# Kernel optimization log

Measured on AMD Instinct MI355X. Metric: run time of the kernel, lower is better.

The kernel has to match this reference:

```python
import jax, jax.numpy as jnp
import numpy as np

B, N, C_IN = 8, 8192, 64
M, K, RADIUS = 1024, 64, 0.2
MLP = [64, 64, 128]


def _fps(pts, m):
    """Iterative farthest point sampling. pts: [N,3] -> [m] int32 indices."""
    n = pts.shape[0]

    def step(carry, _):
        dists, last = carry
        d = jnp.sum((pts - pts[last]) ** 2, axis=-1)          # [N]
        dists = jnp.minimum(dists, d)
        nxt = jnp.argmax(dists).astype(jnp.int32)
        return (dists, nxt), nxt

    init = (jnp.full((n,), 1e10, pts.dtype), jnp.int32(0))
    _, idx = jax.lax.scan(step, init, None, length=m - 1)
    return jnp.concatenate([jnp.zeros((1,), jnp.int32), idx])


def _ball_query(new_xyz, xyz, radius, k):
    """new_xyz: [B,3,M], xyz: [B,3,N] -> [B,M,K] neighbor indices.
    First k points within radius (in index order); padded with first hit."""
    d2 = (jnp.sum(new_xyz ** 2, 1)[:, :, None] + jnp.sum(xyz ** 2, 1)[:, None, :]
          - 2.0 * jnp.einsum('bcm,bcn->bmn', new_xyz, xyz))   # [B,M,N]
    mask = d2 < radius * radius
    # stable argsort of ~mask puts indices of in-radius points first, in order
    order = jnp.argsort(jnp.where(mask, 0, 1).astype(jnp.int32), axis=-1)[..., :k]
    count = jnp.sum(mask, axis=-1)                             # [B,M]
    valid = jnp.arange(k)[None, None, :] < count[..., None]
    return jnp.where(valid, order, order[..., :1])


def _group(x, idx):
    """x: [B,C,N], idx: [B,...] -> [B,C,...] gathered along N."""
    return jax.vmap(lambda a, i: a[:, i])(x, idx)


def _forward(xyz, feature, params):
    # FPS centroid indices (torch runs under no_grad -> stop_gradient)
    pts = jax.lax.stop_gradient(jnp.transpose(xyz, (0, 2, 1)))  # [B,N,3]
    cidx = jax.vmap(lambda p: _fps(p, M))(pts)                  # [B,M]
    new_xyz = _group(xyz, cidx)                                 # [B,3,M]
    nidx = _ball_query(jax.lax.stop_gradient(new_xyz),
                       jax.lax.stop_gradient(xyz), RADIUS, K)   # [B,M,K]
    gxyz = _group(xyz, nidx) - new_xyz[..., None]               # [B,3,M,K]
    x = jnp.concatenate([gxyz, _group(feature, nidx)], axis=1)  # [B,3+C,M,K]
    # SharedMLP: 1x1 conv2d + BN (folded to per-channel scale/bias) + ReLU
    for w, s, b in params:
        x = jax.nn.relu(jnp.einsum('oi,bimk->bomk', w, x)
                        * s[:, None, None] + b[:, None, None])
    return new_xyz, jnp.max(x, axis=3)                          # [B,3,M], [B,128,M]


def setup_inputs() -> dict:
    key = jax.random.key(0)
    ks = jax.random.split(key, 5)
    inp = {
        'xyz': jax.random.normal(ks[0], (B, 3, N), jnp.float32),
        'feature': jax.random.normal(ks[1], (B, C_IN, N), jnp.float32),
    }
    prev = C_IN + 3  # use_xyz=True
    for li, co in enumerate(MLP):
        inp[f'w{li}'] = jax.random.normal(ks[2 + li], (co, prev), jnp.float32) / np.sqrt(prev).astype(np.float32)
        inp[f's{li}'] = jnp.ones((co,), jnp.float32)
        inp[f'b{li}'] = jnp.zeros((co,), jnp.float32)
        prev = co
    return inp


def reference(xyz, feature, w0, s0, b0, w1, s1, b1, w2, s2, b2):
    return _forward(xyz, feature, ((w0, s0, b0), (w1, s1, b1), (w2, s2, b2)))
```

## Files before the change

### kernel.cpp

```cpp
#include <hip/hip_runtime.h>


#define B_ 8
#define N_ 8192
#define M_ 1024
#define K_ 64
#define FTW 68

template <int CTRL>
__device__ __forceinline__ unsigned long long dpp_key(unsigned long long k) {
  int lo = __builtin_amdgcn_update_dpp(0, (int)(unsigned int)k, CTRL, 0xF, 0xF, true);
  int hi = __builtin_amdgcn_update_dpp(0, (int)(unsigned int)(k >> 32), CTRL, 0xF, 0xF, true);
  unsigned long long o = ((unsigned long long)(unsigned int)hi << 32) | (unsigned int)lo;
  return o > k ? o : k;
}

template <int CTRL>
__device__ __forceinline__ float dpp_fmax(float v) {
  int o = __builtin_amdgcn_update_dpp(0, __float_as_int(v), CTRL, 0xF, 0xF, true);
  return fmaxf(v, __int_as_float(o));
}
__device__ __forceinline__ float wave_fmax63(float v) {
  v = dpp_fmax<0xB1>(v);
  v = dpp_fmax<0x4E>(v);
  v = dpp_fmax<0x141>(v);
  v = dpp_fmax<0x140>(v);
  v = dpp_fmax<0x142>(v);
  v = dpp_fmax<0x143>(v);
  return v;
}

__global__ __launch_bounds__(256, 1) void fps_ft_kernel(const float* __restrict__ xyz,
                                                        const float* __restrict__ feat,
                                                        float* __restrict__ ft,
                                                        float* __restrict__ nxyz) {
#pragma clang fp contract(off)
  if (blockIdx.x >= 8) {
    const int nb = gridDim.x - 8;
    const int total = B_ * N_ * FTW;
    for (int idx = (blockIdx.x - 8) * 256 + threadIdx.x; idx < total; idx += nb * 256) {
      int c = idx % FTW;
      int bn = idx / FTW;
      int n = bn & (N_ - 1);
      int b = bn >> 13;
      float v;
      if (c < 3) v = xyz[(b * 3 + c) * N_ + n];
      else if (c < 67) v = feat[(b * 64 + (c - 3)) * N_ + n];
      else v = 0.f;
      ft[idx] = v;
    }
    return;
  }

  __shared__ float4 pts4[N_];
  __shared__ unsigned long long cand[2][16];
  __shared__ int scidx[M_];
  const int b = blockIdx.x;
  const int t = threadIdx.x;
  const int lane = t & 63;
  const int wid = t >> 6;
  const float* xb = xyz + b * 3 * N_;

  for (int n = t; n < N_; n += 256) {
    pts4[n] = make_float4(xb[n], xb[N_ + n], xb[2 * N_ + n], 0.f);
  }

  const int base = t * 32;
  float px[32], py[32], pz[32], mind[32];
#pragma unroll
  for (int j = 0; j < 32; ++j) {
    px[j] = xb[base + j];
    py[j] = xb[N_ + base + j];
    pz[j] = xb[2 * N_ + base + j];
    mind[j] = 1e10f;
  }
  float xl = xb[0], yl = xb[N_], zl = xb[2 * N_];
  if (t == 0) scidx[0] = 0;
  __syncthreads();

  for (int i = 1; i < M_; ++i) {
    float bestv = -1.f;
    int bl = 0;
#pragma unroll
    for (int j = 0; j < 32; ++j) {
      float dx = __fsub_rn(px[j], xl);
      float dy = __fsub_rn(py[j], yl);
      float dz = __fsub_rn(pz[j], zl);
      float d = __fadd_rn(__fadd_rn(__fmul_rn(dx, dx), __fmul_rn(dy, dy)), __fmul_rn(dz, dz));
      float md = fminf(mind[j], d);
      mind[j] = md;
      if (md > bestv) { bestv = md; bl = j; }
    }
    unsigned long long key =
        ((unsigned long long)__float_as_uint(bestv) << 32) | (unsigned int)(~(base + bl));
    key = dpp_key<0xB1>(key);
    key = dpp_key<0x4E>(key);
    key = dpp_key<0x141>(key);
    key = dpp_key<0x140>(key);
    if ((lane & 15) == 0) cand[i & 1][wid * 4 + (lane >> 4)] = key;
    __syncthreads();
    unsigned long long gk = cand[i & 1][lane & 15];
    gk = dpp_key<0xB1>(gk);
    gk = dpp_key<0x4E>(gk);
    gk = dpp_key<0x141>(gk);
    gk = dpp_key<0x140>(gk);
    const int gi = (int)(~(unsigned int)gk);
    if (t == 0) scidx[i] = gi;
    float4 cc = pts4[gi];
    xl = cc.x; yl = cc.y; zl = cc.z;
  }
  __syncthreads();
  for (int q = t; q < M_; q += 256) {
    int ci = scidx[q];
    float4 c = pts4[ci];
    nxyz[b * 3 * M_ + q] = c.x;
    nxyz[b * 3 * M_ + M_ + q] = c.y;
    nxyz[b * 3 * M_ + 2 * M_ + q] = c.z;
  }
}

__global__ __launch_bounds__(256) void ballq_kernel(const float* __restrict__ xyz,
                                                    const float* __restrict__ nxyz,
                                                    int* __restrict__ nidx) {
  const int lane = threadIdx.x & 63;
  const int g = blockIdx.x * 4 + (threadIdx.x >> 6);
  const int b = g >> 10;
  const int m = g & (M_ - 1);
  const float* xb = xyz + b * 3 * N_;
  const float cx = nxyz[b * 3 * M_ + m];
  const float cy = nxyz[b * 3 * M_ + M_ + m];
  const float cz = nxyz[b * 3 * M_ + 2 * M_ + m];
  const float nc = __fadd_rn(__fadd_rn(__fmul_rn(cx, cx), __fmul_rn(cy, cy)), __fmul_rn(cz, cz));
  int cnt = 0;
  int first = 0;
  int* slot = nidx + (g << 6);
  for (int basei = 0; basei < N_ && cnt < K_; basei += 64) {
    const int n = basei + lane;
    float p_x = xb[n], p_y = xb[N_ + n], p_z = xb[2 * N_ + n];
    float pn = __fadd_rn(__fadd_rn(__fmul_rn(p_x, p_x), __fmul_rn(p_y, p_y)), __fmul_rn(p_z, p_z));
    float dt = __fadd_rn(__fadd_rn(__fmul_rn(cx, p_x), __fmul_rn(cy, p_y)), __fmul_rn(cz, p_z));
    float d2 = __fsub_rn(__fadd_rn(nc, pn), __fmul_rn(2.f, dt));
    bool inr = d2 < 0.04f;
    unsigned long long mk = __ballot(inr);
    if (cnt == 0 && mk != 0ull) first = basei + (__ffsll((long long)mk) - 1);
    int pos = cnt + (int)__popcll(mk & ((1ull << lane) - 1ull));
    if (inr && pos < K_) slot[pos] = n;
    cnt += (int)__popcll(mk);
  }
  if (cnt > K_) cnt = K_;
  if (lane >= cnt) slot[lane] = first;
}

template <bool USE_FT>
__global__ __launch_bounds__(64, 4) void mlp_kernel(
    const float* __restrict__ ft, const float* __restrict__ xyz, const float* __restrict__ feat,
    const int* __restrict__ nidx, const float* __restrict__ nxyz,
    const float* __restrict__ w0, const float* __restrict__ s0, const float* __restrict__ b0,
    const float* __restrict__ w1, const float* __restrict__ s1, const float* __restrict__ b1,
    const float* __restrict__ w2, const float* __restrict__ s2, const float* __restrict__ b2,
    float* __restrict__ out2) {
  __shared__ float ylds[64 * 33];
  const int g = blockIdx.x;
  const int b = g >> 10;
  const int m = g & (M_ - 1);
  const int lane = threadIdx.x;
  const int n = nidx[(g << 6) + lane];
  const float cx = nxyz[b * 3 * M_ + m];
  const float cy = nxyz[b * 3 * M_ + M_ + m];
  const float cz = nxyz[b * 3 * M_ + 2 * M_ + m];

  float x0[67];
  if (USE_FT) {
    const float4* row = (const float4*)(ft + (size_t)((b << 13) + n) * FTW);
    float f[FTW];
#pragma unroll
    for (int q = 0; q < 17; ++q) {
      float4 v = row[q];
      f[q * 4 + 0] = v.x; f[q * 4 + 1] = v.y; f[q * 4 + 2] = v.z; f[q * 4 + 3] = v.w;
    }
    x0[0] = f[0] - cx; x0[1] = f[1] - cy; x0[2] = f[2] - cz;
#pragma unroll
    for (int c = 3; c < 67; ++c) x0[c] = f[c];
  } else {
    const float* xb = xyz + b * 3 * N_;
    x0[0] = xb[n] - cx; x0[1] = xb[N_ + n] - cy; x0[2] = xb[2 * N_ + n] - cz;
#pragma unroll
    for (int c = 0; c < 64; ++c) x0[3 + c] = feat[((b << 6) + c) * N_ + n];
  }

  float x1[64];
#pragma unroll
  for (int h = 0; h < 2; ++h) {
#pragma unroll 2
    for (int oo = 0; oo < 32; oo += 4) {
      const int o = h * 32 + oo;
      const float* wr = w0 + o * 67;
      float a0 = 0.f, a1 = 0.f, a2 = 0.f, a3 = 0.f;
#pragma unroll
      for (int ci = 0; ci < 67; ++ci) {
        float xvv = x0[ci];
        a0 = fmaf(wr[ci], xvv, a0);
        a1 = fmaf(wr[67 + ci], xvv, a1);
        a2 = fmaf(wr[134 + ci], xvv, a2);
        a3 = fmaf(wr[201 + ci], xvv, a3);
      }
      ylds[lane * 33 + oo + 0] = fmaxf(fmaf(a0, s0[o + 0], b0[o + 0]), 0.f);
      ylds[lane * 33 + oo + 1] = fmaxf(fmaf(a1, s0[o + 1], b0[o + 1]), 0.f);
      ylds[lane * 33 + oo + 2] = fmaxf(fmaf(a2, s0[o + 2], b0[o + 2]), 0.f);
      ylds[lane * 33 + oo + 3] = fmaxf(fmaf(a3, s0[o + 3], b0[o + 3]), 0.f);
    }
#pragma unroll
    for (int c = 0; c < 32; ++c) x1[h * 32 + c] = ylds[lane * 33 + c];
  }

  float x2[64];
#pragma unroll
  for (int h = 0; h < 2; ++h) {
#pragma unroll 2
    for (int oo = 0; oo < 32; oo += 4) {
      const int o = h * 32 + oo;
      const float* wr = w1 + o * 64;
      float a0 = 0.f, a1 = 0.f, a2 = 0.f, a3 = 0.f;
#pragma unroll
      for (int ci = 0; ci < 64; ++ci) {
        float xvv = x1[ci];
        a0 = fmaf(wr[ci], xvv, a0);
        a1 = fmaf(wr[64 + ci], xvv, a1);
        a2 = fmaf(wr[128 + ci], xvv, a2);
        a3 = fmaf(wr[192 + ci], xvv, a3);
      }
      ylds[lane * 33 + oo + 0] = fmaxf(fmaf(a0, s1[o + 0], b1[o + 0]), 0.f);
      ylds[lane * 33 + oo + 1] = fmaxf(fmaf(a1, s1[o + 1], b1[o + 1]), 0.f);
      ylds[lane * 33 + oo + 2] = fmaxf(fmaf(a2, s1[o + 2], b1[o + 2]), 0.f);
      ylds[lane * 33 + oo + 3] = fmaxf(fmaf(a3, s1[o + 3], b1[o + 3]), 0.f);
    }
#pragma unroll
    for (int c = 0; c < 32; ++c) x2[h * 32 + c] = ylds[lane * 33 + c];
  }

  float* outbm = out2 + (size_t)(b * 128) * M_ + m;
#pragma unroll 2
  for (int o = 0; o < 128; o += 4) {
    const float* wr = w2 + o * 64;
    float a0 = 0.f, a1 = 0.f, a2 = 0.f, a3 = 0.f;
#pragma unroll
    for (int ci = 0; ci < 64; ++ci) {
      float xvv = x2[ci];
      a0 = fmaf(wr[ci], xvv, a0);
      a1 = fmaf(wr[64 + ci], xvv, a1);
      a2 = fmaf(wr[128 + ci], xvv, a2);
      a3 = fmaf(wr[192 + ci], xvv, a3);
    }
    float v0 = fmaxf(fmaf(a0, s2[o + 0], b2[o + 0]), 0.f);
    float v1 = fmaxf(fmaf(a1, s2[o + 1], b2[o + 1]), 0.f);
    float v2 = fmaxf(fmaf(a2, s2[o + 2], b2[o + 2]), 0.f);
    float v3 = fmaxf(fmaf(a3, s2[o + 3], b2[o + 3]), 0.f);
    v0 = wave_fmax63(v0);
    v1 = wave_fmax63(v1);
    v2 = wave_fmax63(v2);
    v3 = wave_fmax63(v3);
    float g0 = __int_as_float(__builtin_amdgcn_readlane(__float_as_int(v0), 63));
    float g1 = __int_as_float(__builtin_amdgcn_readlane(__float_as_int(v1), 63));
    float g2 = __int_as_float(__builtin_amdgcn_readlane(__float_as_int(v2), 63));
    float g3 = __int_as_float(__builtin_amdgcn_readlane(__float_as_int(v3), 63));
    if (lane == ((o + 0) & 63)) outbm[(o + 0) * M_] = g0;
    if (lane == ((o + 1) & 63)) outbm[(o + 1) * M_] = g1;
    if (lane == ((o + 2) & 63)) outbm[(o + 2) * M_] = g2;
    if (lane == ((o + 3) & 63)) outbm[(o + 3) * M_] = g3;
  }
}

extern "C" void kernel_launch(void* const* d_in, const int* in_sizes, int n_in,
                              void* d_out, int out_size, void* d_ws, size_t ws_size,
                              hipStream_t stream) {
  const float* xyz = (const float*)d_in[0];
  const float* feat = (const float*)d_in[1];
  const float* w0 = (const float*)d_in[2];
  const float* s0 = (const float*)d_in[3];
  const float* b0 = (const float*)d_in[4];
  const float* w1 = (const float*)d_in[5];
  const float* s1 = (const float*)d_in[6];
  const float* b1 = (const float*)d_in[7];
  const float* w2 = (const float*)d_in[8];
  const float* s2 = (const float*)d_in[9];
  const float* b2 = (const float*)d_in[10];

  float* nxyz = (float*)d_out;
  float* out2 = (float*)d_out + B_ * 3 * M_;

  const size_t nidx_bytes = (size_t)B_ * M_ * K_ * sizeof(int);
  const size_t ft_bytes = (size_t)B_ * N_ * FTW * sizeof(float);
  int* nidx = (int*)d_ws;
  float* ft = (float*)((char*)d_ws + nidx_bytes);
  const bool use_ft = ws_size >= nidx_bytes + ft_bytes;

  hipLaunchKernelGGL(fps_ft_kernel, dim3(use_ft ? 64 : 8), dim3(256), 0, stream,
                     xyz, feat, ft, nxyz);
  hipLaunchKernelGGL(ballq_kernel, dim3(B_ * M_ / 4), dim3(256), 0, stream, xyz, nxyz, nidx);
  if (use_ft) {
    hipLaunchKernelGGL((mlp_kernel<true>), dim3(B_ * M_), dim3(64), 0, stream,
                       ft, xyz, feat, nidx, nxyz, w0, s0, b0, w1, s1, b1, w2, s2, b2, out2);
  } else {
    hipLaunchKernelGGL((mlp_kernel<false>), dim3(B_ * M_), dim3(64), 0, stream,
                       ft, xyz, feat, nidx, nxyz, w0, s0, b0, w1, s1, b1, w2, s2, b2, out2);
  }
}
```

Before: 1.282 ms.

## Transpose MLP mapping: lanes own output channels, weights in registers, activations in LDS

After: 1.253 ms. -2.3%, faster.

```diff
diff --git a/kernel.cpp b/kernel.cpp
--- a/kernel.cpp
+++ b/kernel.cpp
@@ -32,10 +32,18 @@
 
 __global__ __launch_bounds__(256, 1) void fps_ft_kernel(const float* __restrict__ xyz,
                                                         const float* __restrict__ feat,
+                                                        const float* __restrict__ w0,
+                                                        float* __restrict__ w0pad,
                                                         float* __restrict__ ft,
                                                         float* __restrict__ nxyz) {
 #pragma clang fp contract(off)
   if (blockIdx.x >= 8) {
+    if (blockIdx.x == 8) {
+      for (int i = threadIdx.x; i < 64 * FTW; i += 256) {
+        int o = i / FTW, c = i % FTW;
+        w0pad[i] = (c < 67) ? w0[o * 67 + c] : 0.f;
+      }
+    }
     const int nb = gridDim.x - 8;
     const int total = B_ * N_ * FTW;
     for (int idx = (blockIdx.x - 8) * 256 + threadIdx.x; idx < total; idx += nb * 256) {
@@ -151,9 +159,139 @@
   if (lane >= cnt) slot[lane] = first;
 }
 
-template <bool USE_FT>
-__global__ __launch_bounds__(64, 4) void mlp_kernel(
-    const float* __restrict__ ft, const float* __restrict__ xyz, const float* __restrict__ feat,
+__global__ __launch_bounds__(64, 3) void mlp_t_kernel(
+    const float* __restrict__ ft, const float* __restrict__ w0pad,
+    const int* __restrict__ nidx, const float* __restrict__ nxyz,
+    const float* __restrict__ s0, const float* __restrict__ b0,
+    const float* __restrict__ w1, const float* __restrict__ s1, const float* __restrict__ b1,
+    const float* __restrict__ w2, const float* __restrict__ s2, const float* __restrict__ b2,
+    float* __restrict__ out2) {
+  __shared__ float xls[64 * FTW];
+  const int g = blockIdx.x;
+  const int b = g >> 10;
+  const int m = g & (M_ - 1);
+  const int lane = threadIdx.x;
+
+  const float cx = nxyz[b * 3 * M_ + m];
+  const float cy = nxyz[b * 3 * M_ + M_ + m];
+  const float cz = nxyz[b * 3 * M_ + 2 * M_ + m];
+
+  {
+    const int nk = nidx[(g << 6) + lane];
+    const float4* src = (const float4*)(ft + (size_t)((b << 13) + nk) * FTW);
+    float4* dst = (float4*)(xls + lane * FTW);
+    float4 v0 = src[0];
+    v0.x -= cx; v0.y -= cy; v0.z -= cz;
+    dst[0] = v0;
+#pragma unroll
+    for (int q = 1; q < 17; ++q) dst[q] = src[q];
+  }
+
+  float w0r[FTW];
+  {
+    const float4* wp = (const float4*)(w0pad + lane * FTW);
+#pragma unroll
+    for (int q = 0; q < 17; ++q) {
+      float4 wv = wp[q];
+      w0r[4 * q + 0] = wv.x; w0r[4 * q + 1] = wv.y;
+      w0r[4 * q + 2] = wv.z; w0r[4 * q + 3] = wv.w;
+    }
+  }
+  const float s0l = s0[lane], b0l = b0[lane];
+  for (int k = 0; k < 64; k += 2) {
+    const float4* rowA = (const float4*)(xls + k * FTW);
+    const float4* rowB = (const float4*)(xls + (k + 1) * FTW);
+    float aA = 0.f, aB = 0.f;
+#pragma unroll
+    for (int q = 0; q < 17; ++q) {
+      float4 xa = rowA[q];
+      float4 xbv = rowB[q];
+      aA = fmaf(w0r[4 * q + 0], xa.x, aA);
+      aA = fmaf(w0r[4 * q + 1], xa.y, aA);
+      aA = fmaf(w0r[4 * q + 2], xa.z, aA);
+      aA = fmaf(w0r[4 * q + 3], xa.w, aA);
+      aB = fmaf(w0r[4 * q + 0], xbv.x, aB);
+      aB = fmaf(w0r[4 * q + 1], xbv.y, aB);
+      aB = fmaf(w0r[4 * q + 2], xbv.z, aB);
+      aB = fmaf(w0r[4 * q + 3], xbv.w, aB);
+    }
+    xls[k * FTW + lane] = fmaxf(fmaf(aA, s0l, b0l), 0.f);
+    xls[(k + 1) * FTW + lane] = fmaxf(fmaf(aB, s0l, b0l), 0.f);
+  }
+
+  float w1r[64];
+  {
+    const float4* wp = (const float4*)(w1 + lane * 64);
+#pragma unroll
+    for (int q = 0; q < 16; ++q) {
+      float4 wv = wp[q];
+      w1r[4 * q + 0] = wv.x; w1r[4 * q + 1] = wv.y;
+      w1r[4 * q + 2] = wv.z; w1r[4 * q + 3] = wv.w;
+    }
+  }
+  const float s1l = s1[lane], b1l = b1[lane];
+  for (int k = 0; k < 64; k += 2) {
+    const float4* rowA = (const float4*)(xls + k * FTW);
+    const float4* rowB = (const float4*)(xls + (k + 1) * FTW);
+    float aA = 0.f, aB = 0.f;
+#pragma unroll
+    for (int q = 0; q < 16; ++q) {
+      float4 xa = rowA[q];
+      float4 xbv = rowB[q];
+      aA = fmaf(w1r[4 * q + 0], xa.x, aA);
+      aA = fmaf(w1r[4 * q + 1], xa.y, aA);
+      aA = fmaf(w1r[4 * q + 2], xa.z, aA);
+      aA = fmaf(w1r[4 * q + 3], xa.w, aA);
+      aB = fmaf(w1r[4 * q + 0], xbv.x, aB);
+      aB = fmaf(w1r[4 * q + 1], xbv.y, aB);
+      aB = fmaf(w1r[4 * q + 2], xbv.z, aB);
+      aB = fmaf(w1r[4 * q + 3], xbv.w, aB);
+    }
+    xls[k * FTW + lane] = fmaxf(fmaf(aA, s1l, b1l), 0.f);
+    xls[(k + 1) * FTW + lane] = fmaxf(fmaf(aB, s1l, b1l), 0.f);
+  }
+
+  float w2a[64], w2b[64];
+  {
+    const float4* wpa = (const float4*)(w2 + lane * 64);
+    const float4* wpb = (const float4*)(w2 + (64 + lane) * 64);
+#pragma unroll
+    for (int q = 0; q < 16; ++q) {
+      float4 wv = wpa[q];
+      w2a[4 * q + 0] = wv.x; w2a[4 * q + 1] = wv.y;
+      w2a[4 * q + 2] = wv.z; w2a[4 * q + 3] = wv.w;
+      float4 wu = wpb[q];
+      w2b[4 * q + 0] = wu.x; w2b[4 * q + 1] = wu.y;
+      w2b[4 * q + 2] = wu.z; w2b[4 * q + 3] = wu.w;
+    }
+  }
+  const float s2a = s2[lane], b2a = b2[lane];
+  const float s2b = s2[64 + lane], b2b = b2[64 + lane];
+  float vmaxA = 0.f, vmaxB = 0.f;
+  for (int k = 0; k < 64; ++k) {
+    const float4* row = (const float4*)(xls + k * FTW);
+    float aA = 0.f, aB = 0.f;
+#pragma unroll
+    for (int q = 0; q < 16; ++q) {
+      float4 xa = row[q];
+      aA = fmaf(w2a[4 * q + 0], xa.x, aA);
+      aA = fmaf(w2a[4 * q + 1], xa.y, aA);
+      aA = fmaf(w2a[4 * q + 2], xa.z, aA);
+      aA = fmaf(w2a[4 * q + 3], xa.w, aA);
+      aB = fmaf(w2b[4 * q + 0], xa.x, aB);
+      aB = fmaf(w2b[4 * q + 1], xa.y, aB);
+      aB = fmaf(w2b[4 * q + 2], xa.z, aB);
+      aB = fmaf(w2b[4 * q + 3], xa.w, aB);
+    }
+    vmaxA = fmaxf(vmaxA, fmaxf(fmaf(aA, s2a, b2a), 0.f));
+    vmaxB = fmaxf(vmaxB, fmaxf(fmaf(aB, s2b, b2b), 0.f));
+  }
+  out2[(size_t)((b << 7) + lane) * M_ + m] = vmaxA;
+  out2[(size_t)((b << 7) + 64 + lane) * M_ + m] = vmaxB;
+}
+
+__global__ __launch_bounds__(64, 4) void mlp_kernel_fb(
+    const float* __restrict__ xyz, const float* __restrict__ feat,
     const int* __restrict__ nidx, const float* __restrict__ nxyz,
     const float* __restrict__ w0, const float* __restrict__ s0, const float* __restrict__ b0,
     const float* __restrict__ w1, const float* __restrict__ s1, const float* __restrict__ b1,
@@ -170,23 +308,10 @@
   const float cz = nxyz[b * 3 * M_ + 2 * M_ + m];
 
   float x0[67];
-  if (USE_FT) {
-    const float4* row = (const float4*)(ft + (size_t)((b << 13) + n) * FTW);
-    float f[FTW];
-#pragma unroll
-    for (int q = 0; q < 17; ++q) {
-      float4 v = row[q];
-      f[q * 4 + 0] = v.x; f[q * 4 + 1] = v.y; f[q * 4 + 2] = v.z; f[q * 4 + 3] = v.w;
-    }
-    x0[0] = f[0] - cx; x0[1] = f[1] - cy; x0[2] = f[2] - cz;
-#pragma unroll
-    for (int c = 3; c < 67; ++c) x0[c] = f[c];
-  } else {
-    const float* xb = xyz + b * 3 * N_;
-    x0[0] = xb[n] - cx; x0[1] = xb[N_ + n] - cy; x0[2] = xb[2 * N_ + n] - cz;
-#pragma unroll
-    for (int c = 0; c < 64; ++c) x0[3 + c] = feat[((b << 6) + c) * N_ + n];
-  }
+  const float* xb = xyz + b * 3 * N_;
+  x0[0] = xb[n] - cx; x0[1] = xb[N_ + n] - cy; x0[2] = xb[2 * N_ + n] - cz;
+#pragma unroll
+  for (int c = 0; c < 64; ++c) x0[3 + c] = feat[((b << 6) + c) * N_ + n];
 
   float x1[64];
 #pragma unroll
@@ -289,19 +414,21 @@
   float* out2 = (float*)d_out + B_ * 3 * M_;
 
   const size_t nidx_bytes = (size_t)B_ * M_ * K_ * sizeof(int);
+  const size_t w0p_bytes = (size_t)64 * FTW * sizeof(float);
   const size_t ft_bytes = (size_t)B_ * N_ * FTW * sizeof(float);
   int* nidx = (int*)d_ws;
-  float* ft = (float*)((char*)d_ws + nidx_bytes);
-  const bool use_ft = ws_size >= nidx_bytes + ft_bytes;
+  float* w0pad = (float*)((char*)d_ws + nidx_bytes);
+  float* ft = (float*)((char*)d_ws + nidx_bytes + w0p_bytes);
+  const bool use_ft = ws_size >= nidx_bytes + w0p_bytes + ft_bytes;
 
   hipLaunchKernelGGL(fps_ft_kernel, dim3(use_ft ? 64 : 8), dim3(256), 0, stream,
-                     xyz, feat, ft, nxyz);
+                     xyz, feat, w0, w0pad, ft, nxyz);
   hipLaunchKernelGGL(ballq_kernel, dim3(B_ * M_ / 4), dim3(256), 0, stream, xyz, nxyz, nidx);
   if (use_ft) {
-    hipLaunchKernelGGL((mlp_kernel<true>), dim3(B_ * M_), dim3(64), 0, stream,
-                       ft, xyz, feat, nidx, nxyz, w0, s0, b0, w1, s1, b1, w2, s2, b2, out2);
+    hipLaunchKernelGGL(mlp_t_kernel, dim3(B_ * M_), dim3(64), 0, stream,
+                       ft, w0pad, nidx, nxyz, s0, b0, w1, s1, b1, w2, s2, b2, out2);
   } else {
-    hipLaunchKernelGGL((mlp_kernel<false>), dim3(B_ * M_), dim3(64), 0, stream,
-                       ft, xyz, feat, nidx, nxyz, w0, s0, b0, w1, s1, b1, w2, s2, b2, out2);
-  }
-}
+    hipLaunchKernelGGL(mlp_kernel_fb, dim3(B_ * M_), dim3(64), 0, stream,
+                       xyz, feat, nidx, nxyz, w0, s0, b0, w1, s1, b1, w2, s2, b2, out2);
+  }
+}
```
